# Performance work log

Hardware: AMD Instinct MI355X
Metric: run time of the kernel (lower is better)

Reference implementation:

```python
import jax, jax.numpy as jnp
import numpy as np

NUM_HEADS = 16
ROPE_BASE = 10000.0


def apply_rope(x):
    # x: [B, T, H, D]; torchtune-style interleaved-pair RoPE, positions 0..T-1
    B, T, H, D = x.shape
    inv_freq = 1.0 / (ROPE_BASE ** (jnp.arange(0, D, 2, dtype=jnp.float32) / D))  # [D/2]
    pos = jnp.arange(T, dtype=jnp.float32)
    freqs = pos[:, None] * inv_freq[None, :]              # [T, D/2]
    cos = jnp.cos(freqs)[None, :, None, :].astype(x.dtype)
    sin = jnp.sin(freqs)[None, :, None, :].astype(x.dtype)
    x1 = x[..., 0::2]
    x2 = x[..., 1::2]
    o1 = x1 * cos - x2 * sin
    o2 = x2 * cos + x1 * sin
    return jnp.stack([o1, o2], axis=-1).reshape(B, T, H, D)


def setup_inputs() -> dict:
    key = jax.random.key(0)
    k1, k2, k3 = jax.random.split(key, 3)
    B, T, C = 2, 8192, 1024
    x = jax.random.normal(k1, (B, T, C), dtype=jnp.float32)
    # torch Linear weight layout [out_features, in_features]; fan-in scaling
    Wqkv = jax.random.normal(k2, (3 * C, C), dtype=jnp.float32) * (C ** -0.5)
    Wout = jax.random.normal(k3, (C, C), dtype=jnp.float32) * (C ** -0.5)
    return {"x": x, "Wqkv": Wqkv, "Wout": Wout}


def reference(x, Wqkv, Wout):
    B, T, C = x.shape
    H = NUM_HEADS
    D = C // H
    qkv = (x @ Wqkv.T).reshape(B, T, 3, H, D)
    q, k, v = qkv[:, :, 0], qkv[:, :, 1], qkv[:, :, 2]   # each [B, T, H, D]
    q = apply_rope(q)
    k = apply_rope(k)
    # Faithful to source: SDPA is called on [B, T, H, D] WITHOUT transposing,
    # so torch attends over the heads axis (L = H) with (B, T) as batch dims.
    scale = 1.0 / jnp.sqrt(jnp.asarray(D, dtype=x.dtype))
    scores = jnp.einsum('btqd,btkd->btqk', q, k) * scale  # [B, T, H, H]
    attn = jax.nn.softmax(scores, axis=-1)
    out = jnp.einsum('btqk,btkd->btqd', attn, v)          # [B, T, H, D]
    # Replicate attn_output.transpose(1, 2).contiguous().view(B, T, C)
    out = out.transpose(0, 2, 1, 3).reshape(B, T, C)
    return out @ Wout.T
```

## Files before the change

### kernel.cpp

```cpp
#include <hip/hip_runtime.h>
#include <stdint.h>

#define TT 8192
#define BT 16384
#define MCH 8192

typedef __attribute__((ext_vector_type(8))) __bf16 bf16x8;
typedef __attribute__((ext_vector_type(4))) __bf16 bf16x4;
typedef __attribute__((ext_vector_type(4))) short short4v;
typedef __attribute__((ext_vector_type(4))) float floatx4;

__device__ __forceinline__ float bf2f(unsigned short h) {
  union { unsigned u; float f; } x; x.u = ((unsigned)h) << 16; return x.f;
}
__device__ __forceinline__ unsigned short f2bf(float f) {
  union { float f; unsigned u; } x; x.f = f;
  unsigned r = (x.u + 0x7fffu + ((x.u >> 16) & 1u)) >> 16;
  return (unsigned short)r;
}
__device__ __forceinline__ void async16(const void* g, void* l) {
  __builtin_amdgcn_global_load_lds(
      (__attribute__((address_space(1))) void*)g,
      (__attribute__((address_space(3))) void*)l, 16, 0, 0);
}

__global__ __launch_bounds__(256) void cvt_f2b(
    const float* __restrict__ src, unsigned short* __restrict__ dst, int n4) {
  const int i = blockIdx.x * 256 + threadIdx.x;
  if (i < n4) {
    const float4 f = ((const float4*)src)[i];
    union { uint2 u2; unsigned short s[4]; } o;
    o.s[0] = f2bf(f.x); o.s[1] = f2bf(f.y);
    o.s[2] = f2bf(f.z); o.s[3] = f2bf(f.w);
    ((uint2*)dst)[i] = o.u2;
  }
}

__global__ __launch_bounds__(256) void prep_k(
    const float* __restrict__ Wqkv, const float* __restrict__ Wout,
    unsigned short* __restrict__ Wqkvb, unsigned short* __restrict__ Woutb,
    float2* __restrict__ tab) {
  const int bx = blockIdx.x;
  const int tid = threadIdx.x;
  if (bx < 1024) {
    const int i = bx * 256 + tid;
    const int t = i >> 5, p = i & 31;
    const float f = (float)t * exp2f((float)p * -0.41524101186092f);
    float s, c;
    sincosf(f, &s, &c);
    tab[i] = make_float2(c, s);
  } else {
    const float* src;
    unsigned short* dst;
    int i;
    if (bx < 4096) { src = Wqkv; dst = Wqkvb; i = (bx - 1024) * 256 + tid; }
    else           { src = Wout; dst = Woutb; i = (bx - 4096) * 256 + tid; }
    const float4 f = ((const float4*)src)[i];
    union { uint2 u2; unsigned short s[4]; } o;
    o.s[0] = f2bf(f.x); o.s[1] = f2bf(f.y);
    o.s[2] = f2bf(f.z); o.s[3] = f2bf(f.w);
    ((uint2*)dst)[i] = o.u2;
  }
}

template <bool CF32>
__global__ __launch_bounds__(512, 4) void gemm_k32(
    const unsigned short* __restrict__ A,
    const unsigned short* __restrict__ W,
    void* __restrict__ C,
    int M, int N, int K)
{
  __shared__ __align__(16) unsigned short sm[2][(256 + 128) * 32];

  const int tid  = threadIdx.x;
  const int lane = tid & 63;
  const int wid  = tid >> 6;
  const int wr   = wid >> 1;
  const int wc   = wid & 1;
  const int lm   = lane & 15;
  const int kg   = lane >> 4;
  const int cxor = (lm >> 1) & 3;

  const int nb  = N >> 7;
  const int cpx = (int)gridDim.x >> 3;
  const int bid = blockIdx.x;
  const int swz = (bid & 7) * cpx + (bid >> 3);
  const int bm  = swz / nb;
  const int bn  = swz % nb;

  const int NT = K >> 5;

  const int sr  = lane >> 2;
  const int scb = lane & 3;
  const unsigned short* gsrc0;
  const unsigned short* gsrc1;
  const unsigned short* gsrc2;
  {
    const int r0 = wid * 16 + sr;
    const int r1 = 128 + r0;
    const int rB = wid * 16 + sr;
    gsrc0 = A + (size_t)(bm * 256 + r0) * (size_t)K + ((scb ^ ((r0 >> 1) & 3)) << 3);
    gsrc1 = A + (size_t)(bm * 256 + r1) * (size_t)K + ((scb ^ ((r1 >> 1) & 3)) << 3);
    gsrc2 = W + (size_t)(bn * 128 + rB) * (size_t)K + ((scb ^ ((rB >> 1) & 3)) << 3);
  }
  const int ld0 = wid * 1024;
  const int ld1 = 8192 + wid * 1024;
  const int ld2 = 16384 + wid * 1024;

  auto stage_tile = [&](int tt) {
    char* lb = (char*)sm[tt & 1];
    const size_t koff = (size_t)tt << 5;
    async16(gsrc0 + koff, lb + ld0);
    async16(gsrc1 + koff, lb + ld1);
    async16(gsrc2 + koff, lb + ld2);
  };

  floatx4 acc[4][4];
  floatx4 z = {0.f, 0.f, 0.f, 0.f};
#pragma unroll
  for (int i = 0; i < 4; ++i)
#pragma unroll
    for (int j = 0; j < 4; ++j) acc[i][j] = z;

  stage_tile(0);
  stage_tile(1);
  asm volatile("s_waitcnt vmcnt(3)" ::: "memory");
  __builtin_amdgcn_s_barrier();
  __builtin_amdgcn_sched_barrier(0);

  for (int t = 0; t < NT; ++t) {
    const unsigned short* Ab = sm[t & 1];
    const unsigned short* Bb = Ab + 256 * 32;

    bf16x8 af[4], bfr[4];
#pragma unroll
    for (int i = 0; i < 4; ++i) {
      const int rr = wr * 64 + i * 16 + lm;
      af[i] = *(const bf16x8*)(Ab + rr * 32 + ((kg ^ cxor) << 3));
    }
#pragma unroll
    for (int j = 0; j < 4; ++j) {
      const int rr = wc * 64 + j * 16 + lm;
      bfr[j] = *(const bf16x8*)(Bb + rr * 32 + ((kg ^ cxor) << 3));
    }

    __builtin_amdgcn_s_barrier();
    asm volatile("s_waitcnt lgkmcnt(0)" ::: "memory");
    __builtin_amdgcn_sched_barrier(0);

    if (t + 2 < NT) stage_tile(t + 2);

    __builtin_amdgcn_s_setprio(1);
#pragma unroll
    for (int i = 0; i < 4; ++i)
#pragma unroll
      for (int j = 0; j < 4; ++j)
        acc[i][j] = __builtin_amdgcn_mfma_f32_16x16x32_bf16(
            af[i], bfr[j], acc[i][j], 0, 0, 0);
    __builtin_amdgcn_s_setprio(0);

    if (t + 1 < NT) {
      if (t + 2 < NT)
        asm volatile("s_waitcnt vmcnt(3)" ::: "memory");
      else
        asm volatile("s_waitcnt vmcnt(0)" ::: "memory");
      __builtin_amdgcn_s_barrier();
      __builtin_amdgcn_sched_barrier(0);
    }
  }

#pragma unroll
  for (int i = 0; i < 4; ++i) {
    const int row0 = bm * 256 + wr * 64 + i * 16 + kg * 4;
#pragma unroll
    for (int j = 0; j < 4; ++j) {
      const int col = bn * 128 + wc * 64 + j * 16 + lm;
#pragma unroll
      for (int r = 0; r < 4; ++r) {
        if (CF32)
          ((float*)C)[(size_t)(row0 + r) * N + col] = acc[i][j][r];
        else
          ((unsigned short*)C)[(size_t)(row0 + r) * N + col] = f2bf(acc[i][j][r]);
      }
    }
  }
}

#if defined(__has_builtin)
#if __has_builtin(__builtin_amdgcn_mfma_f32_16x16x16_bf16)
#define PV_MFMA 1
#define PV_MFMA_CALL(a, b, c) __builtin_amdgcn_mfma_f32_16x16x16_bf16( \
    *(bf16x4*)&(a), *(bf16x4*)&(b), (c), 0, 0, 0)
#elif __has_builtin(__builtin_amdgcn_mfma_f32_16x16x16bf16_1k)
#define PV_MFMA 1
#define PV_MFMA_CALL(a, b, c) __builtin_amdgcn_mfma_f32_16x16x16bf16_1k( \
    (a), (b), (c), 0, 0, 0)
#else
#define PV_MFMA 0
#endif
#else
#define PV_MFMA 0
#endif

__global__ __launch_bounds__(128) void attn_rope_k(
    const unsigned short* __restrict__ qkv,
    const float2* __restrict__ tab,
    unsigned short* __restrict__ Y,
    int base)
{
  __shared__ __align__(16) unsigned short sQKV[2][2][3 * 16 * 72];
#if !PV_MFMA
  __shared__ float sP[2][2][256];
#endif

  const int wave = threadIdx.x >> 6;
  const int lane = threadIdx.x & 63;
  const int ml0  = blockIdx.x * 4 + wave * 2;
  const int lm   = lane & 15;
  const int quad = lane >> 4;

  int tA[2], bA[2];
#pragma unroll
  for (int tk = 0; tk < 2; ++tk) {
    const int m = base + ml0 + tk;
    tA[tk] = m & (TT - 1);
    bA[tk] = m >> 13;
  }

#pragma unroll
  for (int tk = 0; tk < 2; ++tk) {
    const uint4* row = (const uint4*)(qkv + (size_t)(ml0 + tk) * 3072);
    const int t = tA[tk];
    unsigned short* QB = sQKV[wave][tk];
#pragma unroll
    for (int i = 0; i < 6; ++i) {
      const int c = lane + 64 * i;
      union { uint4 u4; unsigned short s[8]; } cv;
      cv.u4 = row[c];
      const int n0   = c * 8;
      const int part = n0 >> 10;
      const int h    = (n0 >> 6) & 15;
      const int d0   = n0 & 63;
      if (part < 2) {
        float f[8];
#pragma unroll
        for (int j = 0; j < 8; ++j) f[j] = bf2f(cv.s[j]);
        const int p0 = d0 >> 1;
        const float4 csA = *(const float4*)(tab + (t << 5) + p0);
        const float4 csB = *(const float4*)(tab + (t << 5) + p0 + 2);
        const float cs[4] = {csA.x, csA.z, csB.x, csB.z};
        const float sn[4] = {csA.y, csA.w, csB.y, csB.w};
#pragma unroll
        for (int j = 0; j < 4; ++j) {
          const float x1 = f[2 * j], x2 = f[2 * j + 1];
          cv.s[2 * j]     = f2bf(x1 * cs[j] - x2 * sn[j]);
          cv.s[2 * j + 1] = f2bf(x2 * cs[j] + x1 * sn[j]);
        }
      }
      unsigned short* dst = QB + part * (16 * 72) + h * 72 + d0;
      *(uint4*)dst = cv.u4;
    }
  }
  asm volatile("s_waitcnt lgkmcnt(0)" ::: "memory");
  __builtin_amdgcn_sched_barrier(0);

  floatx4 accS[2];
#pragma unroll
  for (int tk = 0; tk < 2; ++tk) {
    floatx4 a = {0.f, 0.f, 0.f, 0.f};
    const unsigned short* QB = sQKV[wave][tk];
    const unsigned short* KB = QB + 16 * 72;
#pragma unroll
    for (int half = 0; half < 2; ++half) {
      const bf16x8 kf = *(const bf16x8*)(KB + lm * 72 + half * 32 + quad * 8);
      const bf16x8 qf = *(const bf16x8*)(QB + lm * 72 + half * 32 + quad * 8);
      a = __builtin_amdgcn_mfma_f32_16x16x32_bf16(kf, qf, a, 0, 0, 0);
    }
    accS[tk] = a;
  }

  float s4[2][4], inv[2];
#pragma unroll
  for (int tk = 0; tk < 2; ++tk) {
    float mx = -1e30f;
#pragma unroll
    for (int j = 0; j < 4; ++j) {
      s4[tk][j] = accS[tk][j] * 0.125f;
      mx = fmaxf(mx, s4[tk][j]);
    }
    mx = fmaxf(mx, __shfl_xor(mx, 16, 64));
    mx = fmaxf(mx, __shfl_xor(mx, 32, 64));
    float sum = 0.f;
#pragma unroll
    for (int j = 0; j < 4; ++j) { s4[tk][j] = __expf(s4[tk][j] - mx); sum += s4[tk][j]; }
    sum += __shfl_xor(sum, 16, 64);
    sum += __shfl_xor(sum, 32, 64);
    inv[tk] = 1.0f / sum;
  }

#if PV_MFMA
  union { short4v v; unsigned short s[4]; } pf[2];
#pragma unroll
  for (int tk = 0; tk < 2; ++tk)
#pragma unroll
    for (int j = 0; j < 4; ++j) {
      const float p = s4[tk][j] * inv[tk];
      pf[tk].s[j] = p == 0.f ? 0 : f2bf(p);
    }
#pragma unroll
  for (int dtile = 0; dtile < 4; ++dtile) {
#pragma unroll
    for (int tk = 0; tk < 2; ++tk) {
      const unsigned short* VB = sQKV[wave][tk] + 2 * 16 * 72;
      union { short4v v; unsigned short s[4]; } vf;
#pragma unroll
      for (int j = 0; j < 4; ++j)
        vf.s[j] = VB[(quad * 4 + j) * 72 + dtile * 16 + lm];
      floatx4 accO = {0.f, 0.f, 0.f, 0.f};
      accO = PV_MFMA_CALL(pf[tk].v, vf.v, accO);
      const int t = tA[tk];
      const int col = (t & 15) * 64 + dtile * 16 + lm;
#pragma unroll
      for (int r = 0; r < 4; ++r) {
        const size_t rr = (size_t)bA[tk] * TT + (size_t)(quad * 4 + r) * 512 + (t >> 4);
        Y[rr * 1024 + col] = f2bf(accO[r]);
      }
    }
  }
#else
#pragma unroll
  for (int tk = 0; tk < 2; ++tk) {
    float* P = sP[wave][tk];
    const unsigned short* VB = sQKV[wave][tk] + 2 * 16 * 72;
    const int t = tA[tk];
#pragma unroll
    for (int j = 0; j < 4; ++j) P[(quad * 4 + j) * 16 + lm] = s4[tk][j] * inv[tk];
    asm volatile("s_waitcnt lgkmcnt(0)" ::: "memory");
    __builtin_amdgcn_sched_barrier(0);
    float o[16];
#pragma unroll
    for (int dd = 0; dd < 16; ++dd) o[dd] = 0.f;
#pragma unroll
    for (int kh = 0; kh < 16; ++kh) {
      const float a = P[kh * 16 + lm];
      union { uint4 u4; unsigned short s[8]; } v0, v1;
      v0.u4 = *(const uint4*)(VB + kh * 72 + quad * 16);
      v1.u4 = *(const uint4*)(VB + kh * 72 + quad * 16 + 8);
#pragma unroll
      for (int dd = 0; dd < 8; ++dd) {
        o[dd]     += a * bf2f(v0.s[dd]);
        o[dd + 8] += a * bf2f(v1.s[dd]);
      }
    }
    const size_t rr = (size_t)bA[tk] * TT + (size_t)lm * 512 + (t >> 4);
    unsigned short* yp = Y + rr * 1024 + (t & 15) * 64 + quad * 16;
    union { uint4 u4; unsigned short s[8]; } o1, o2;
#pragma unroll
    for (int dd = 0; dd < 8; ++dd) o1.s[dd] = f2bf(o[dd]);
#pragma unroll
    for (int dd = 0; dd < 8; ++dd) o2.s[dd] = f2bf(o[8 + dd]);
    ((uint4*)yp)[0] = o1.u4;
    ((uint4*)yp)[1] = o2.u4;
  }
#endif
}

extern "C" void kernel_launch(void* const* d_in, const int* in_sizes, int n_in,
                              void* d_out, int out_size, void* d_ws, size_t ws_size,
                              hipStream_t stream) {
  const float* x    = (const float*)d_in[0];
  const float* Wqkv = (const float*)d_in[1];
  const float* Wout = (const float*)d_in[2];
  float* out = (float*)d_out;

  unsigned short* Y     = (unsigned short*)d_ws;
  unsigned short* Wqkvb = Y + (size_t)BT * 1024;
  unsigned short* Woutb = Wqkvb + (size_t)3072 * 1024;
  unsigned short* xb    = Woutb + (size_t)1024 * 1024;
  unsigned short* qkvC  = (unsigned short*)d_out;
  float2* tab           = (float2*)((char*)d_out + (size_t)52 * 1024 * 1024);

  prep_k<<<dim3(5120), dim3(256), 0, stream>>>(Wqkv, Wout, Wqkvb, Woutb, tab);

  for (int base = 0; base < BT; base += MCH) {
    cvt_f2b<<<dim3(MCH * 1024 / 4 / 256), dim3(256), 0, stream>>>(
        x + (size_t)base * 1024, xb, MCH * 1024 / 4);
    gemm_k32<false><<<dim3((MCH / 256) * (3072 / 128)), dim3(512), 0, stream>>>(
        xb, Wqkvb, qkvC, MCH, 3072, 1024);
    attn_rope_k<<<dim3(MCH / 4), dim3(128), 0, stream>>>(qkvC, tab, Y, base);
  }

  gemm_k32<true><<<dim3((BT / 256) * (1024 / 128)), dim3(512), 0, stream>>>(
      Y, Woutb, out, BT, 1024, 1024);
}
```

Baseline: 310.1 us.

## Keep RoPE'd Q/K in registers via ds_bpermute, stage only V in LDS

Restructures the attention+RoPE kernel so each lane loads its whole row slice into registers up front, applies RoPE with a single per-lane cos/sin load, and feeds the QK MFMA through ds_bpermute lane shuffles instead of writing Q and K to shared memory. Only V is staged in LDS, which cuts LDS footprint and traffic. The block grows to 256 threads with an occupancy hint, and priority is raised around the MFMA section. Register pressure rises from holding twelve uint4 plus tables, and the bpermutes add cross-lane instruction cost.

```diff
diff --git a/kernel.cpp b/kernel.cpp
--- a/kernel.cpp
+++ b/kernel.cpp
@@ -202,123 +202,117 @@
 #define PV_MFMA 0
 #endif
 
-__global__ __launch_bounds__(128) void attn_rope_k(
+__global__ __launch_bounds__(256, 4) void attn_rope_k(
     const unsigned short* __restrict__ qkv,
     const float2* __restrict__ tab,
     unsigned short* __restrict__ Y,
     int base)
 {
-  __shared__ __align__(16) unsigned short sQKV[2][2][3 * 16 * 72];
+  __shared__ __align__(16) unsigned short sV[4][16 * 72];
 #if !PV_MFMA
-  __shared__ float sP[2][2][256];
+  __shared__ float sP[4][256];
 #endif
 
   const int wave = threadIdx.x >> 6;
   const int lane = threadIdx.x & 63;
-  const int ml0  = blockIdx.x * 4 + wave * 2;
   const int lm   = lane & 15;
   const int quad = lane >> 4;
-
+  const int ml0  = blockIdx.x * 8 + wave * 2;
+  unsigned short* VB = sV[wave];
+
+  const int hlo = lane >> 3;
+  const int d0  = (lane & 7) * 8;
+  const int p0  = d0 >> 1;
+
+  uint4 R[2][6];
+  float4 CS[2][2];
   int tA[2], bA[2];
 #pragma unroll
   for (int tk = 0; tk < 2; ++tk) {
     const int m = base + ml0 + tk;
     tA[tk] = m & (TT - 1);
     bA[tk] = m >> 13;
+    const uint4* row = (const uint4*)(qkv + (size_t)(ml0 + tk) * 3072);
+#pragma unroll
+    for (int i = 0; i < 6; ++i) R[tk][i] = row[lane + 64 * i];
+    CS[tk][0] = *(const float4*)(tab + (tA[tk] << 5) + p0);
+    CS[tk][1] = *(const float4*)(tab + (tA[tk] << 5) + p0 + 2);
   }
 
 #pragma unroll
   for (int tk = 0; tk < 2; ++tk) {
-    const uint4* row = (const uint4*)(qkv + (size_t)(ml0 + tk) * 3072);
     const int t = tA[tk];
-    unsigned short* QB = sQKV[wave][tk];
-#pragma unroll
-    for (int i = 0; i < 6; ++i) {
-      const int c = lane + 64 * i;
+    const float cs[4] = {CS[tk][0].x, CS[tk][0].z, CS[tk][1].x, CS[tk][1].z};
+    const float sn[4] = {CS[tk][0].y, CS[tk][0].w, CS[tk][1].y, CS[tk][1].w};
+
+    uint4 P[4];
+#pragma unroll
+    for (int i = 0; i < 4; ++i) {
       union { uint4 u4; unsigned short s[8]; } cv;
-      cv.u4 = row[c];
-      const int n0   = c * 8;
-      const int part = n0 >> 10;
-      const int h    = (n0 >> 6) & 15;
-      const int d0   = n0 & 63;
-      if (part < 2) {
-        float f[8];
-#pragma unroll
-        for (int j = 0; j < 8; ++j) f[j] = bf2f(cv.s[j]);
-        const int p0 = d0 >> 1;
-        const float4 csA = *(const float4*)(tab + (t << 5) + p0);
-        const float4 csB = *(const float4*)(tab + (t << 5) + p0 + 2);
-        const float cs[4] = {csA.x, csA.z, csB.x, csB.z};
-        const float sn[4] = {csA.y, csA.w, csB.y, csB.w};
-#pragma unroll
-        for (int j = 0; j < 4; ++j) {
-          const float x1 = f[2 * j], x2 = f[2 * j + 1];
-          cv.s[2 * j]     = f2bf(x1 * cs[j] - x2 * sn[j]);
-          cv.s[2 * j + 1] = f2bf(x2 * cs[j] + x1 * sn[j]);
-        }
-      }
-      unsigned short* dst = QB + part * (16 * 72) + h * 72 + d0;
-      *(uint4*)dst = cv.u4;
-    }
-  }
-  asm volatile("s_waitcnt lgkmcnt(0)" ::: "memory");
-  __builtin_amdgcn_sched_barrier(0);
-
-  floatx4 accS[2];
-#pragma unroll
-  for (int tk = 0; tk < 2; ++tk) {
-    floatx4 a = {0.f, 0.f, 0.f, 0.f};
-    const unsigned short* QB = sQKV[wave][tk];
-    const unsigned short* KB = QB + 16 * 72;
+      cv.u4 = R[tk][i];
+      float f[8];
+#pragma unroll
+      for (int j = 0; j < 8; ++j) f[j] = bf2f(cv.s[j]);
+#pragma unroll
+      for (int j = 0; j < 4; ++j) {
+        const float x1 = f[2 * j], x2 = f[2 * j + 1];
+        cv.s[2 * j]     = f2bf(x1 * cs[j] - x2 * sn[j]);
+        cv.s[2 * j + 1] = f2bf(x2 * cs[j] + x1 * sn[j]);
+      }
+      P[i] = cv.u4;
+    }
+
+    *(uint4*)(VB + hlo * 72 + d0)       = R[tk][4];
+    *(uint4*)(VB + (8 + hlo) * 72 + d0) = R[tk][5];
+
+    __builtin_amdgcn_s_setprio(1);
+    floatx4 accS = {0.f, 0.f, 0.f, 0.f};
 #pragma unroll
     for (int half = 0; half < 2; ++half) {
-      const bf16x8 kf = *(const bf16x8*)(KB + lm * 72 + half * 32 + quad * 8);
-      const bf16x8 qf = *(const bf16x8*)(QB + lm * 72 + half * 32 + quad * 8);
-      a = __builtin_amdgcn_mfma_f32_16x16x32_bf16(kf, qf, a, 0, 0, 0);
-    }
-    accS[tk] = a;
-  }
-
-  float s4[2][4], inv[2];
-#pragma unroll
-  for (int tk = 0; tk < 2; ++tk) {
+      const int bpi = (((lm & 7) * 8) + half * 4 + quad) * 4;
+      union { int w[4]; bf16x8 v; } kf, qf;
+#pragma unroll
+      for (int w = 0; w < 4; ++w) {
+        const int q0 = __builtin_amdgcn_ds_bpermute(bpi, (int)(&P[0].x)[w]);
+        const int q1 = __builtin_amdgcn_ds_bpermute(bpi, (int)(&P[1].x)[w]);
+        qf.w[w] = lm < 8 ? q0 : q1;
+        const int k0 = __builtin_amdgcn_ds_bpermute(bpi, (int)(&P[2].x)[w]);
+        const int k1 = __builtin_amdgcn_ds_bpermute(bpi, (int)(&P[3].x)[w]);
+        kf.w[w] = lm < 8 ? k0 : k1;
+      }
+      accS = __builtin_amdgcn_mfma_f32_16x16x32_bf16(kf.v, qf.v, accS, 0, 0, 0);
+    }
+
+    float s4[4];
     float mx = -1e30f;
 #pragma unroll
-    for (int j = 0; j < 4; ++j) {
-      s4[tk][j] = accS[tk][j] * 0.125f;
-      mx = fmaxf(mx, s4[tk][j]);
-    }
+    for (int j = 0; j < 4; ++j) { s4[j] = accS[j] * 0.125f; mx = fmaxf(mx, s4[j]); }
     mx = fmaxf(mx, __shfl_xor(mx, 16, 64));
     mx = fmaxf(mx, __shfl_xor(mx, 32, 64));
     float sum = 0.f;
 #pragma unroll
-    for (int j = 0; j < 4; ++j) { s4[tk][j] = __expf(s4[tk][j] - mx); sum += s4[tk][j]; }
+    for (int j = 0; j < 4; ++j) { s4[j] = __expf(s4[j] - mx); sum += s4[j]; }
     sum += __shfl_xor(sum, 16, 64);
     sum += __shfl_xor(sum, 32, 64);
-    inv[tk] = 1.0f / sum;
-  }
+    const float inv = 1.0f / sum;
 
 #if PV_MFMA
-  union { short4v v; unsigned short s[4]; } pf[2];
-#pragma unroll
-  for (int tk = 0; tk < 2; ++tk)
-#pragma unroll
-    for (int j = 0; j < 4; ++j) {
-      const float p = s4[tk][j] * inv[tk];
-      pf[tk].s[j] = p == 0.f ? 0 : f2bf(p);
-    }
-#pragma unroll
-  for (int dtile = 0; dtile < 4; ++dtile) {
-#pragma unroll
-    for (int tk = 0; tk < 2; ++tk) {
-      const unsigned short* VB = sQKV[wave][tk] + 2 * 16 * 72;
+    union { short4v v; unsigned short s[4]; } pf;
+#pragma unroll
+    for (int j = 0; j < 4; ++j) pf.s[j] = f2bf(s4[j] * inv);
+    unsigned short vs[16];
+#pragma unroll
+    for (int dtile = 0; dtile < 4; ++dtile)
+#pragma unroll
+      for (int j = 0; j < 4; ++j)
+        vs[dtile * 4 + j] = VB[(quad * 4 + j) * 72 + dtile * 16 + lm];
+#pragma unroll
+    for (int dtile = 0; dtile < 4; ++dtile) {
       union { short4v v; unsigned short s[4]; } vf;
 #pragma unroll
-      for (int j = 0; j < 4; ++j)
-        vf.s[j] = VB[(quad * 4 + j) * 72 + dtile * 16 + lm];
+      for (int j = 0; j < 4; ++j) vf.s[j] = vs[dtile * 4 + j];
       floatx4 accO = {0.f, 0.f, 0.f, 0.f};
-      accO = PV_MFMA_CALL(pf[tk].v, vf.v, accO);
-      const int t = tA[tk];
+      accO = PV_MFMA_CALL(pf.v, vf.v, accO);
       const int col = (t & 15) * 64 + dtile * 16 + lm;
 #pragma unroll
       for (int r = 0; r < 4; ++r) {
@@ -326,15 +320,12 @@
         Y[rr * 1024 + col] = f2bf(accO[r]);
       }
     }
-  }
+    __builtin_amdgcn_s_setprio(0);
 #else
-#pragma unroll
-  for (int tk = 0; tk < 2; ++tk) {
-    float* P = sP[wave][tk];
-    const unsigned short* VB = sQKV[wave][tk] + 2 * 16 * 72;
-    const int t = tA[tk];
-#pragma unroll
-    for (int j = 0; j < 4; ++j) P[(quad * 4 + j) * 16 + lm] = s4[tk][j] * inv[tk];
+    __builtin_amdgcn_s_setprio(0);
+    float* Pp = sP[wave];
+#pragma unroll
+    for (int j = 0; j < 4; ++j) Pp[(quad * 4 + j) * 16 + lm] = s4[j] * inv;
     asm volatile("s_waitcnt lgkmcnt(0)" ::: "memory");
     __builtin_amdgcn_sched_barrier(0);
     float o[16];
@@ -342,7 +333,7 @@
     for (int dd = 0; dd < 16; ++dd) o[dd] = 0.f;
 #pragma unroll
     for (int kh = 0; kh < 16; ++kh) {
-      const float a = P[kh * 16 + lm];
+      const float a = Pp[kh * 16 + lm];
       union { uint4 u4; unsigned short s[8]; } v0, v1;
       v0.u4 = *(const uint4*)(VB + kh * 72 + quad * 16);
       v1.u4 = *(const uint4*)(VB + kh * 72 + quad * 16 + 8);
@@ -361,8 +352,8 @@
     for (int dd = 0; dd < 8; ++dd) o2.s[dd] = f2bf(o[8 + dd]);
     ((uint4*)yp)[0] = o1.u4;
     ((uint4*)yp)[1] = o2.u4;
-  }
 #endif
+  }
 }
 
 extern "C" void kernel_launch(void* const* d_in, const int* in_sizes, int n_in,
@@ -387,7 +378,7 @@
         x + (size_t)base * 1024, xb, MCH * 1024 / 4);
     gemm_k32<false><<<dim3((MCH / 256) * (3072 / 128)), dim3(512), 0, stream>>>(
         xb, Wqkvb, qkvC, MCH, 3072, 1024);
-    attn_rope_k<<<dim3(MCH / 4), dim3(128), 0, stream>>>(qkvC, tab, Y, base);
+    attn_rope_k<<<dim3(MCH / 8), dim3(256), 0, stream>>>(qkvC, tab, Y, base);
   }
 
   gemm_k32<true><<<dim3((BT / 256) * (1024 / 128)), dim3(512), 0, stream>>>(
```

Result: no change. 312.5 us (+0.8%).
